# Kernel tuning notes

Hardware: AMD Instinct MI355X
Metric: run time of the kernel (lower is better)

Reference implementation:

```python
import jax, jax.numpy as jnp
import numpy as np

SAMPLE_RATE = 16000
N_TRANSIENTS = 20
TRANSIENT_SAMPLES = 1600  # int(0.1 s * 16000 Hz)
BATCH = 64
MAX_TRANSIENTS = 256
AUDIO_LEN = 160000  # 10 s @ 16 kHz


def setup_inputs() -> dict:
    key = jax.random.key(0)
    k1, k2, k3, k4 = jax.random.split(key, 4)
    # timings in seconds, sorted per batch (as in generate_random_transients)
    transient_timings = jnp.sort(
        jax.random.uniform(k1, (BATCH, MAX_TRANSIENTS), dtype=jnp.float32) * 9.0, axis=1)
    transient_ids = jax.random.randint(k2, (BATCH, MAX_TRANSIENTS), 0, N_TRANSIENTS)
    transient_gains = 0.1 + 0.9 * jax.random.uniform(k3, (BATCH, MAX_TRANSIENTS), dtype=jnp.float32)
    transient_templates = jax.random.normal(k4, (N_TRANSIENTS, TRANSIENT_SAMPLES), dtype=jnp.float32)
    return {
        "transient_timings": transient_timings,
        "transient_ids": transient_ids,
        "transient_gains": transient_gains,
        "transient_templates": transient_templates,
        "audio_length": AUDIO_LEN,
    }


def reference(transient_timings, transient_ids, transient_gains, transient_templates, audio_length):
    n_tr, L = transient_templates.shape
    # start sample of each transient (timings are non-negative, so floor == int())
    t_sample = jnp.floor(transient_timings * SAMPLE_RATE).astype(jnp.int32)  # [B, T]
    # skip conditions from the original loop: gain <= 0, id >= n_transients, start >= audio_length
    valid = (transient_gains > 0) & (transient_ids < n_tr) & (t_sample < audio_length)
    # gather templates: [B, T, L]
    tmpl = transient_templates[jnp.clip(transient_ids, 0, n_tr - 1)]
    vals = tmpl * (transient_gains * valid.astype(transient_gains.dtype))[..., None]
    # destination positions: [B, T, L]; positions >= audio_length are dropped (truncation)
    pos = t_sample[..., None] + jnp.arange(L, dtype=jnp.int32)

    def scatter_one(p, v):
        # p, v: [T, L] -> scatter-add into [audio_length]
        return jnp.zeros((audio_length,), v.dtype).at[p.reshape(-1)].add(
            v.reshape(-1), mode='drop')

    return jax.vmap(scatter_one)(pos, vals)  # [B, audio_length]
```

## Files before the change

kernel.cpp:

```cpp
#include <hip/hip_runtime.h>


constexpr int SR    = 16000;
constexpr int TL    = 1600;
constexpr int MAXT  = 256;
constexpr int NTHR  = 256;
constexpr int CHUNK = 1024;

__global__ __launch_bounds__(NTHR)
void transient_gather(const float* __restrict__ timings,
                      const int*   __restrict__ ids,
                      const float* __restrict__ gains,
                      const float* __restrict__ templates,
                      float*       __restrict__ out,
                      int T, int n_tr, int A)
{
    __shared__ int2               s_m[MAXT];
    __shared__ unsigned long long s_mask[NTHR / 64];

    const int b      = blockIdx.y;
    const int chunk0 = blockIdx.x * CHUNK;
    const int tid    = (int)threadIdx.x;

    {
        const float tm = timings[(size_t)b * T + tid];
        const float g  = gains  [(size_t)b * T + tid];
        const int   id = ids    [(size_t)b * T + tid];
        const int   ts = (int)floorf(tm * (float)SR);
        const bool ok  = (g > 0.0f) & (id < n_tr) & (ts < A);
        const int tsc  = min(max(ts, 0), A);
        const int idc  = min(max(id, 0), n_tr - 1);
        s_m[tid] = make_int2((tsc << 8) | idc, ok ? __float_as_int(g) : 0);

        const bool ov = (tsc < chunk0 + CHUNK) && (tsc + TL > chunk0);
        const unsigned long long m = __ballot(ov);
        if ((tid & 63) == 0) s_mask[tid >> 6] = m;
    }
    __syncthreads();

    int lo = T, hi = -1;
#pragma unroll
    for (int w = 0; w < NTHR / 64; ++w) {
        const unsigned long long mw = s_mask[w];
        if (mw) {
            lo = min(lo, w * 64 + (int)__builtin_ctzll(mw));
            hi = max(hi, w * 64 + 63 - (int)__builtin_clzll(mw));
        }
    }

    float acc[4] = {0.f, 0.f, 0.f, 0.f};
    const int off_base = chunk0 + tid;

    for (int j = lo; j <= hi; ++j) {
        const int2  m  = s_m[j];
        const int   ts = m.x >> 8;
        const float g  = __int_as_float(m.y);
        const float* __restrict__ row = templates + (size_t)(m.x & 255) * TL;
        const int off0 = off_base - ts;
#pragma unroll
        for (int k = 0; k < 4; ++k) {
            const int o = off0 + k * NTHR;
            if ((unsigned)o < (unsigned)TL)
                acc[k] += g * row[o];
        }
    }

    float* ob = out + (size_t)b * A + off_base;
#pragma unroll
    for (int k = 0; k < 4; ++k) {
        if (off_base + k * NTHR < A) ob[k * NTHR] = acc[k];
    }
}

extern "C" void kernel_launch(void* const* d_in, const int* in_sizes, int n_in,
                              void* d_out, int out_size, void* d_ws, size_t ws_size,
                              hipStream_t stream) {
    const float* timings   = (const float*)d_in[0];
    const int*   ids       = (const int*)  d_in[1];
    const float* gains     = (const float*)d_in[2];
    const float* templates = (const float*)d_in[3];
    float*       out       = (float*)d_out;

    const int T    = MAXT;
    const int B    = in_sizes[0] / T;
    const int n_tr = in_sizes[3] / TL;
    const int A    = out_size / B;

    dim3 grid((A + CHUNK - 1) / CHUNK, B), block(NTHR);
    transient_gather<<<grid, block, 0, stream>>>(timings, ids, gains, templates, out,
                                                 T, n_tr, A);
}
```

Measured before the change: 26.20 us.

## Switch to per-wavefront persistent chunks with register-resident metadata and readlane broadcast

Each wavefront now owns whole 1024-sample chunks and loops over them persistently, keeping transient metadata in registers and broadcasting it with readlane. This removes the shared memory, the block barrier and the per-block metadata reload. Each lane accumulates 16 outputs instead of 4. A fast path handles transients that fully cover the chunk without bounds masking, and zero-gain transients are skipped. The trade-offs are more registers per lane, fewer wavefronts in flight (8192 in total, each handling one or two chunks), and a serial walk over transients in each wave.

Result: slower. 28.84 us (+10.1%).

```diff
diff --git a/kernel.cpp b/kernel.cpp
--- a/kernel.cpp
+++ b/kernel.cpp
@@ -1,74 +1,98 @@
 #include <hip/hip_runtime.h>
 
 
-constexpr int SR    = 16000;
-constexpr int TL    = 1600;
-constexpr int MAXT  = 256;
-constexpr int NTHR  = 256;
-constexpr int CHUNK = 1024;
+constexpr int SR   = 16000;
+constexpr int TL   = 1600;
+constexpr int MAXT = 256;
+constexpr int CHW  = 1024;
+constexpr int KPL  = 16;
+constexpr int WPB  = 128;
 
-__global__ __launch_bounds__(NTHR)
-void transient_gather(const float* __restrict__ timings,
-                      const int*   __restrict__ ids,
-                      const float* __restrict__ gains,
-                      const float* __restrict__ templates,
-                      float*       __restrict__ out,
-                      int T, int n_tr, int A)
+__global__ __launch_bounds__(256)
+void transient_pw(const float* __restrict__ timings,
+                  const int*   __restrict__ ids,
+                  const float* __restrict__ gains,
+                  const float* __restrict__ templates,
+                  float*       __restrict__ out,
+                  int T, int n_tr, int A, int nchunk)
 {
-    __shared__ int2               s_m[MAXT];
-    __shared__ unsigned long long s_mask[NTHR / 64];
+    const int lane = (int)(threadIdx.x & 63);
+    const int wg   = blockIdx.x * 4 + (int)(threadIdx.x >> 6);
+    const int b    = wg / WPB;
+    const int w    = wg % WPB;
 
-    const int b      = blockIdx.y;
-    const int chunk0 = blockIdx.x * CHUNK;
-    const int tid    = (int)threadIdx.x;
-
-    {
-        const float tm = timings[(size_t)b * T + tid];
-        const float g  = gains  [(size_t)b * T + tid];
-        const int   id = ids    [(size_t)b * T + tid];
+    int   mx[4];
+    float mg[4];
+#pragma unroll
+    for (int q = 0; q < 4; ++q) {
+        const int j    = q * 64 + lane;
+        const float tm = timings[(size_t)b * T + j];
+        const float g  = gains  [(size_t)b * T + j];
+        const int   id = ids    [(size_t)b * T + j];
         const int   ts = (int)floorf(tm * (float)SR);
         const bool ok  = (g > 0.0f) & (id < n_tr) & (ts < A);
         const int tsc  = min(max(ts, 0), A);
         const int idc  = min(max(id, 0), n_tr - 1);
-        s_m[tid] = make_int2((tsc << 8) | idc, ok ? __float_as_int(g) : 0);
-
-        const bool ov = (tsc < chunk0 + CHUNK) && (tsc + TL > chunk0);
-        const unsigned long long m = __ballot(ov);
-        if ((tid & 63) == 0) s_mask[tid >> 6] = m;
-    }
-    __syncthreads();
-
-    int lo = T, hi = -1;
-#pragma unroll
-    for (int w = 0; w < NTHR / 64; ++w) {
-        const unsigned long long mw = s_mask[w];
-        if (mw) {
-            lo = min(lo, w * 64 + (int)__builtin_ctzll(mw));
-            hi = max(hi, w * 64 + 63 - (int)__builtin_clzll(mw));
-        }
+        mx[q] = (tsc << 8) | idc;
+        mg[q] = ok ? g : 0.0f;
     }
 
-    float acc[4] = {0.f, 0.f, 0.f, 0.f};
-    const int off_base = chunk0 + tid;
+    for (int c = w; c < nchunk; c += WPB) {
+        const int chunk0 = c * CHW;
 
-    for (int j = lo; j <= hi; ++j) {
-        const int2  m  = s_m[j];
-        const int   ts = m.x >> 8;
-        const float g  = __int_as_float(m.y);
-        const float* __restrict__ row = templates + (size_t)(m.x & 255) * TL;
-        const int off0 = off_base - ts;
+        int lo = T, hi = -1;
 #pragma unroll
-        for (int k = 0; k < 4; ++k) {
-            const int o = off0 + k * NTHR;
-            if ((unsigned)o < (unsigned)TL)
-                acc[k] += g * row[o];
+        for (int q = 0; q < 4; ++q) {
+            const int ts  = mx[q] >> 8;
+            const bool ov = (ts < chunk0 + CHW) & (ts + TL > chunk0);
+            const unsigned long long m = __ballot(ov);
+            if (m) {
+                lo = min(lo, q * 64 + (int)__builtin_ctzll(m));
+                hi = max(hi, q * 64 + 63 - (int)__builtin_clzll(m));
+            }
         }
-    }
 
-    float* ob = out + (size_t)b * A + off_base;
+        float acc[KPL];
 #pragma unroll
-    for (int k = 0; k < 4; ++k) {
-        if (off_base + k * NTHR < A) ob[k * NTHR] = acc[k];
+        for (int k = 0; k < KPL; ++k) acc[k] = 0.0f;
+
+        for (int j = lo; j <= hi; ++j) {
+            const int q = j >> 6, l = j & 63;
+            int sx; float sg;
+            if (q == 0)      { sx = __builtin_amdgcn_readlane(mx[0], l);
+                               sg = __int_as_float(__builtin_amdgcn_readlane(__float_as_int(mg[0]), l)); }
+            else if (q == 1) { sx = __builtin_amdgcn_readlane(mx[1], l);
+                               sg = __int_as_float(__builtin_amdgcn_readlane(__float_as_int(mg[1]), l)); }
+            else if (q == 2) { sx = __builtin_amdgcn_readlane(mx[2], l);
+                               sg = __int_as_float(__builtin_amdgcn_readlane(__float_as_int(mg[2]), l)); }
+            else             { sx = __builtin_amdgcn_readlane(mx[3], l);
+                               sg = __int_as_float(__builtin_amdgcn_readlane(__float_as_int(mg[3]), l)); }
+            if (sg == 0.0f) continue;
+
+            const int ts = sx >> 8;
+            const float* __restrict__ row = templates + (size_t)(sx & 255) * TL;
+            const int off0 = chunk0 + lane - ts;
+
+            if (ts <= chunk0 && ts + TL >= chunk0 + CHW) {
+#pragma unroll
+                for (int k = 0; k < KPL; ++k)
+                    acc[k] = fmaf(sg, row[off0 + k * 64], acc[k]);
+            } else {
+#pragma unroll
+                for (int k = 0; k < KPL; ++k) {
+                    const int o  = off0 + k * 64;
+                    const int oc = min(max(o, 0), TL - 1);
+                    const float gm = ((unsigned)o < (unsigned)TL) ? sg : 0.0f;
+                    acc[k] = fmaf(gm, row[oc], acc[k]);
+                }
+            }
+        }
+
+        float* ob = out + (size_t)b * A + chunk0 + lane;
+#pragma unroll
+        for (int k = 0; k < KPL; ++k) {
+            if (chunk0 + k * 64 + lane < A) ob[k * 64] = acc[k];
+        }
     }
 }
 
@@ -81,12 +105,13 @@
     const float* templates = (const float*)d_in[3];
     float*       out       = (float*)d_out;
 
-    const int T    = MAXT;
-    const int B    = in_sizes[0] / T;
-    const int n_tr = in_sizes[3] / TL;
-    const int A    = out_size / B;
+    const int T      = MAXT;
+    const int B      = in_sizes[0] / T;
+    const int n_tr   = in_sizes[3] / TL;
+    const int A      = out_size / B;
+    const int nchunk = (A + CHW - 1) / CHW;
 
-    dim3 grid((A + CHUNK - 1) / CHUNK, B), block(NTHR);
-    transient_gather<<<grid, block, 0, stream>>>(timings, ids, gains, templates, out,
-                                                 T, n_tr, A);
+    dim3 grid(B * (WPB / 4)), block(256);
+    transient_pw<<<grid, block, 0, stream>>>(timings, ids, gains, templates, out,
+                                             T, n_tr, A, nchunk);
 }
```
